# Optimization experiments

Measured on AMD Instinct MI355X. Metric: run time of the kernel, lower is better.

Reference implementation:

```python
import jax, jax.numpy as jnp
import numpy as np

H, D = 16, 1024
HD = D // H  # 64

def setup_inputs() -> dict:
    key = jax.random.key(0)
    ks = jax.random.split(key, 11)
    B, S = 2, 2048
    s_in = 1.0 / np.sqrt(D)
    return {
        "V": jax.random.normal(ks[0], (B, S, D), jnp.float32),
        "K": jax.random.normal(ks[1], (B, S, D), jnp.float32),
        "Q": jax.random.normal(ks[2], (B, S, D), jnp.float32),
        # stacked per-head Linear weights, torch layout [out,in] -> [H, HD, D]
        "Wv": jax.random.normal(ks[3], (H, HD, D), jnp.float32) * s_in,
        "bv": jnp.zeros((H, HD), jnp.float32),
        "Wk": jax.random.normal(ks[4], (H, HD, D), jnp.float32) * s_in,
        "bk": jnp.zeros((H, HD), jnp.float32),
        "Wq": jax.random.normal(ks[5], (H, HD, D), jnp.float32) * s_in,
        "bq": jnp.zeros((H, HD), jnp.float32),
        "Wo": jax.random.normal(ks[6], (D, D), jnp.float32) * s_in,
        "bo": jnp.zeros((D,), jnp.float32),
    }

def reference(V, K, Q, Wv, bv, Wk, bk, Wq, bq, Wo, bo):
    scale = HD ** (-0.5)
    # per-head projections fused into one batched GEMM: [B,S,D] x [H,HD,D] -> [B,H,S,HD]
    q = jnp.einsum('bsd,hed->bhse', Q, Wq) + bq[None, :, None, :]
    k = jnp.einsum('bsd,hed->bhse', K, Wk) + bk[None, :, None, :]
    v = jnp.einsum('bsd,hed->bhse', V, Wv) + bv[None, :, None, :]
    # scaled dot-product attention
    scores = jnp.einsum('bhqe,bhke->bhqk', q, k) * scale  # [B,H,S,S]
    p = jax.nn.softmax(scores, axis=-1)
    att = jnp.einsum('bhqk,bhke->bhqe', p, v)  # [B,H,S,HD]
    # concat heads (head 0 first, matching the torch cat order) then output proj
    B, _, S, _ = att.shape
    cat = jnp.transpose(att, (0, 2, 1, 3)).reshape(B, S, H * HD)
    return cat @ Wo.T + bo
```

## Files before the change

### kernel.cpp

```cpp
#include <hip/hip_runtime.h>
#include <cstdint>
#include <cstddef>

typedef __bf16 bf16_t;
typedef bf16_t bf16x8 __attribute__((ext_vector_type(8)));
typedef bf16_t bf16x4 __attribute__((ext_vector_type(4)));
typedef float f32x4 __attribute__((ext_vector_type(4)));

__device__ __forceinline__ void gl_lds16(const void* g, void* l) {
  __builtin_amdgcn_global_load_lds(
      (const __attribute__((address_space(1))) void*)g,
      (__attribute__((address_space(3))) void*)l, 16, 0, 0);
}

__device__ __forceinline__ f32x4 mfma16(bf16x8 a, bf16x8 b, f32x4 c) {
  return __builtin_amdgcn_mfma_f32_16x16x32_bf16(a, b, c, 0, 0, 0);
}

struct CvtWArgs { const float* src[4]; };

__global__ __launch_bounds__(256) void convert_w(CvtWArgs a, bf16_t* __restrict__ dst) {
  unsigned g = blockIdx.x * 256u + threadIdx.x;
  unsigned seg = g >> 17, off = g & 0x1FFFFu;
  const float4* s = (const float4*)a.src[seg] + (size_t)off * 2;
  float4 x0 = s[0], x1 = s[1];
  bf16x8 o;
  o[0] = (bf16_t)x0.x; o[1] = (bf16_t)x0.y; o[2] = (bf16_t)x0.z; o[3] = (bf16_t)x0.w;
  o[4] = (bf16_t)x1.x; o[5] = (bf16_t)x1.y; o[6] = (bf16_t)x1.z; o[7] = (bf16_t)x1.w;
  *(bf16x8*)(dst + (size_t)g * 8) = o;
}

struct ProjArgs {
  const float* A[3]; const bf16_t* W[3]; const float* bias[3];
  bf16_t* out[3]; float scale[3];
};

__global__ __launch_bounds__(256, 3) void gemm_proj(ProjArgs p) {
  __shared__ __attribute__((aligned(16))) unsigned char smem[36864];
  bf16_t* a_s = (bf16_t*)smem;
  bf16_t* b_s = (bf16_t*)(smem + 16384);
  const int K = 1024;
  const int z = blockIdx.z;
  const float*  A = p.A[z] + (size_t)blockIdx.x * 128 * K;
  const bf16_t* W = p.W[z] + (size_t)blockIdx.y * 128 * K;

  const int t = threadIdx.x;
  const int w = t >> 6, l = t & 63;
  const int lq = l >> 4, lr = l & 15;
  const int mq = w & 1, nq = w >> 1;

  f32x4 acc[4][4];
  f32x4 zero = {0.f, 0.f, 0.f, 0.f};
  #pragma unroll
  for (int i = 0; i < 4; i++)
    #pragma unroll
    for (int j = 0; j < 4; j++) acc[i][j] = zero;

  for (int k0 = 0; k0 < K; k0 += 64) {
    __syncthreads();
    float4 av[8];
    #pragma unroll
    for (int f = 0; f < 8; f++) {
      int g = t + f * 256;
      int r = g >> 4, c16 = g & 15;
      av[f] = *(const float4*)(A + (size_t)r * K + k0 + c16 * 4);
    }
    #pragma unroll
    for (int i = 0; i < 4; i++) {
      int g = t + i * 256;
      int r = g >> 3, pc = g & 7;
      int lc = pc ^ (r & 7);
      gl_lds16(W + (size_t)r * K + k0 + lc * 8, b_s + i * 2048 + w * 512);
    }
    #pragma unroll
    for (int f = 0; f < 8; f++) {
      int g = t + f * 256;
      int r = g >> 4, c16 = g & 15;
      int phys = (c16 >> 1) ^ (r & 7);
      bf16x4 bv;
      bv[0] = (bf16_t)av[f].x; bv[1] = (bf16_t)av[f].y;
      bv[2] = (bf16_t)av[f].z; bv[3] = (bf16_t)av[f].w;
      *(bf16x4*)(a_s + r * 64 + phys * 8 + (c16 & 1) * 4) = bv;
    }
    __syncthreads();
    #pragma unroll
    for (int kk = 0; kk < 2; kk++) {
      bf16x8 af[4], bfr[4];
      #pragma unroll
      for (int i = 0; i < 4; i++) {
        int R = mq * 64 + i * 16 + lr;
        int ch = (kk * 4 + lq) ^ (R & 7);
        af[i] = *(const bf16x8*)(a_s + R * 64 + ch * 8);
      }
      #pragma unroll
      for (int j = 0; j < 4; j++) {
        int R = nq * 64 + j * 16 + lr;
        int ch = (kk * 4 + lq) ^ (R & 7);
        bfr[j] = *(const bf16x8*)(b_s + R * 64 + ch * 8);
      }
      #pragma unroll
      for (int i = 0; i < 4; i++)
        #pragma unroll
        for (int j = 0; j < 4; j++)
          acc[i][j] = mfma16(af[i], bfr[j], acc[i][j]);
    }
  }

  const float* bias = p.bias[z];
  const float scale = p.scale[z];
  __syncthreads();
  bf16_t* ts = (bf16_t*)smem;
  #pragma unroll
  for (int i = 0; i < 4; i++) {
    #pragma unroll
    for (int j = 0; j < 4; j++) {
      int nl = nq * 64 + j * 16 + lr;
      float bz = bias[blockIdx.y * 128 + nl];
      #pragma unroll
      for (int r = 0; r < 4; r++) {
        int ml = mq * 64 + i * 16 + lq * 4 + r;
        bf16_t val = (bf16_t)((acc[i][j][r] + bz) * scale);
        if (z == 0) {
          int mlp = (ml & 96) | (((ml >> 2) & 3) << 3) | (((ml >> 4) & 1) << 2) | (ml & 3);
          ts[nl * 136 + mlp] = val;
        } else {
          ts[ml * 136 + nl] = val;
        }
      }
    }
  }
  __syncthreads();
  bf16_t* out = p.out[z];
  const int b = blockIdx.x >> 4, sbase = (blockIdx.x & 15) * 128;
  if (z == 0) {
    #pragma unroll
    for (int ii = 0; ii < 8; ii++) {
      int idx = t * 8 + ii * 2048;
      int rr = idx >> 7, cc = idx & 127;
      int n = blockIdx.y * 128 + rr;
      int h = n >> 6, e = n & 63;
      bf16x8 vq = *(const bf16x8*)(ts + rr * 136 + cc);
      *(bf16x8*)(out + ((size_t)(b * 16 + h) * 64 + e) * 2048 + sbase + cc) = vq;
    }
  } else {
    #pragma unroll
    for (int ii = 0; ii < 8; ii++) {
      int idx = t * 8 + ii * 2048;
      int rr = idx >> 7, cc = idx & 127;
      int n = blockIdx.y * 128 + cc;
      int h = n >> 6, e = n & 63;
      bf16x8 vq = *(const bf16x8*)(ts + rr * 136 + cc);
      *(bf16x8*)(out + ((size_t)(b * 16 + h) * 2048 + sbase + rr) * 64 + e) = vq;
    }
  }
}

__global__ __launch_bounds__(256, 4) void attn(
    const bf16_t* __restrict__ qw, const bf16_t* __restrict__ kw,
    const bf16_t* __restrict__ vtw, bf16_t* __restrict__ att)
{
  __shared__ bf16_t k_s[64 * 64];
  __shared__ bf16_t v_s[64 * 64];
  __shared__ bf16_t qe_s[64 * 72];
  const int bh = blockIdx.x, qt = blockIdx.y;
  const int t = threadIdx.x, w = t >> 6, l = t & 63, lq = l >> 4, lr = l & 15;

  const bf16_t* qbase = qw + ((size_t)bh * 2048 + qt * 64) * 64;
  #pragma unroll
  for (int i = 0; i < 2; i++) {
    int g = t + i * 256;
    int r = g >> 3, pc = g & 7;
    int lc = pc ^ (r & 7);
    gl_lds16(qbase + (size_t)r * 64 + lc * 8, qe_s + i * 2048 + w * 512);
  }
  __syncthreads();
  bf16x8 qf[2];
  #pragma unroll
  for (int kk = 0; kk < 2; kk++) {
    int R = w * 16 + lr;
    int ch = (kk * 4 + lq) ^ (R & 7);
    qf[kk] = *(const bf16x8*)(qe_s + R * 64 + ch * 8);
  }

  f32x4 O[4];
  f32x4 zero = {0.f, 0.f, 0.f, 0.f};
  #pragma unroll
  for (int et = 0; et < 4; et++) O[et] = zero;
  float lsum = 0.f;

  for (int kt = 0; kt < 32; ++kt) {
    __syncthreads();
    const bf16_t* kbase = kw + ((size_t)bh * 2048 + kt * 64) * 64;
    const bf16_t* vbase = vtw + (size_t)bh * 131072 + (size_t)kt * 64;
    #pragma unroll
    for (int i = 0; i < 2; i++) {
      int g = t + i * 256;
      int r = g >> 3, pc = g & 7;
      int lc = pc ^ (r & 7);
      gl_lds16(kbase + (size_t)r * 64 + lc * 8, k_s + i * 2048 + w * 512);
      gl_lds16(vbase + (size_t)r * 2048 + lc * 8, v_s + i * 2048 + w * 512);
    }
    __syncthreads();

    f32x4 sc[4];
    #pragma unroll
    for (int j = 0; j < 4; j++) sc[j] = zero;
    #pragma unroll
    for (int kk = 0; kk < 2; kk++) {
      #pragma unroll
      for (int j = 0; j < 4; j++) {
        int R = j * 16 + lr;
        int ch = (kk * 4 + lq) ^ (R & 7);
        bf16x8 kf = *(const bf16x8*)(k_s + R * 64 + ch * 8);
        sc[j] = mfma16(kf, qf[kk], sc[j]);
      }
    }

    bf16x8 pb[2];
    #pragma unroll
    for (int ks2 = 0; ks2 < 2; ks2++) {
      #pragma unroll
      for (int r = 0; r < 4; r++) {
        float e0 = __expf(sc[2 * ks2][r]);
        float e1 = __expf(sc[2 * ks2 + 1][r]);
        lsum += e0 + e1;
        pb[ks2][r] = (bf16_t)e0;
        pb[ks2][4 + r] = (bf16_t)e1;
      }
    }

    #pragma unroll
    for (int ks2 = 0; ks2 < 2; ks2++) {
      #pragma unroll
      for (int et = 0; et < 4; et++) {
        int R = et * 16 + lr;
        int ch = (ks2 * 4 + lq) ^ (R & 7);
        bf16x8 vf = *(const bf16x8*)(v_s + R * 64 + ch * 8);
        O[et] = mfma16(vf, pb[ks2], O[et]);
      }
    }
  }

  float s = lsum;
  s += __shfl_xor(s, 16);
  s += __shfl_xor(s, 32);
  float rinv = 1.0f / s;

  #pragma unroll
  for (int et = 0; et < 4; et++) {
    bf16x4 pv;
    #pragma unroll
    for (int r = 0; r < 4; r++) pv[r] = (bf16_t)(O[et][r] * rinv);
    *(bf16x4*)(qe_s + (w * 16 + lr) * 72 + et * 16 + lq * 4) = pv;
  }
  __syncthreads();
  const int b = bh >> 4, h = bh & 15;
  #pragma unroll
  for (int i = 0; i < 2; i++) {
    int c = t + i * 256;
    int row = c >> 3, c8 = c & 7;
    bf16x8 vv = *(const bf16x8*)(qe_s + row * 72 + c8 * 8);
    *(bf16x8*)(att + ((size_t)b * 2048 + qt * 64 + row) * 1024 + h * 64 + c8 * 8) = vv;
  }
}

__global__ __launch_bounds__(256, 2) void gemm_out(
    const bf16_t* __restrict__ A, const bf16_t* __restrict__ W,
    const float* __restrict__ bias, float* __restrict__ out)
{
  __shared__ bf16_t a_s[64 * 64];
  __shared__ bf16_t b_s[128 * 64];
  const int K = 1024;
  const bf16_t* Ab = A + (size_t)blockIdx.x * 64 * K;
  const bf16_t* Wb = W + (size_t)blockIdx.y * 128 * K;
  const int t = threadIdx.x, w = t >> 6, l = t & 63, lq = l >> 4, lr = l & 15;
  const int mh = w & 1, nh = w >> 1;

  f32x4 acc[2][4];
  f32x4 zero = {0.f, 0.f, 0.f, 0.f};
  #pragma unroll
  for (int i = 0; i < 2; i++)
    #pragma unroll
    for (int j = 0; j < 4; j++) acc[i][j] = zero;

  for (int k0 = 0; k0 < K; k0 += 64) {
    __syncthreads();
    #pragma unroll
    for (int i = 0; i < 2; i++) {
      int g = t + i * 256;
      int r = g >> 3, pc = g & 7;
      int lc = pc ^ (r & 7);
      gl_lds16(Ab + (size_t)r * K + k0 + lc * 8, a_s + i * 2048 + w * 512);
    }
    #pragma unroll
    for (int i = 0; i < 4; i++) {
      int g = t + i * 256;
      int r = g >> 3, pc = g & 7;
      int lc = pc ^ (r & 7);
      gl_lds16(Wb + (size_t)r * K + k0 + lc * 8, b_s + i * 2048 + w * 512);
    }
    __syncthreads();
    #pragma unroll
    for (int kk = 0; kk < 2; kk++) {
      bf16x8 af[2], bfr[4];
      #pragma unroll
      for (int i = 0; i < 2; i++) {
        int R = mh * 32 + i * 16 + lr;
        int ch = (kk * 4 + lq) ^ (R & 7);
        af[i] = *(const bf16x8*)(a_s + R * 64 + ch * 8);
      }
      #pragma unroll
      for (int j = 0; j < 4; j++) {
        int R = nh * 64 + j * 16 + lr;
        int ch = (kk * 4 + lq) ^ (R & 7);
        bfr[j] = *(const bf16x8*)(b_s + R * 64 + ch * 8);
      }
      #pragma unroll
      for (int i = 0; i < 2; i++)
        #pragma unroll
        for (int j = 0; j < 4; j++)
          acc[i][j] = mfma16(af[i], bfr[j], acc[i][j]);
    }
  }

  #pragma unroll
  for (int i = 0; i < 2; i++) {
    #pragma unroll
    for (int j = 0; j < 4; j++) {
      int col = blockIdx.y * 128 + nh * 64 + j * 16 + lr;
      float bz = bias[col];
      #pragma unroll
      for (int r = 0; r < 4; r++) {
        int row = blockIdx.x * 64 + mh * 32 + i * 16 + lq * 4 + r;
        out[(size_t)row * 1024 + col] = acc[i][j][r] + bz;
      }
    }
  }
}

extern "C" void kernel_launch(void* const* d_in, const int* in_sizes, int n_in,
                              void* d_out, int out_size, void* d_ws, size_t ws_size,
                              hipStream_t stream) {
  (void)in_sizes; (void)n_in; (void)out_size;
  const float* V  = (const float*)d_in[0];
  const float* Kx = (const float*)d_in[1];
  const float* Q  = (const float*)d_in[2];
  const float* Wv = (const float*)d_in[3];
  const float* bv = (const float*)d_in[4];
  const float* Wk = (const float*)d_in[5];
  const float* bk = (const float*)d_in[6];
  const float* Wq = (const float*)d_in[7];
  const float* bq = (const float*)d_in[8];
  const float* Wo = (const float*)d_in[9];
  const float* bo = (const float*)d_in[10];

  const size_t E = 1048576;
  if (ws_size < 20 * E * sizeof(bf16_t)) return;

  bf16_t* ws = (bf16_t*)d_ws;
  bf16_t* cWo   = ws;
  bf16_t* cWv   = ws + E;
  bf16_t* cWk   = ws + 2 * E;
  bf16_t* cWq   = ws + 3 * E;
  bf16_t* q_ws  = ws + 4 * E;
  bf16_t* k_ws  = ws + 8 * E;
  bf16_t* vt_ws = ws + 12 * E;
  bf16_t* att_ws= ws + 16 * E;

  CvtWArgs cw;
  cw.src[0] = Wo; cw.src[1] = Wv; cw.src[2] = Wk; cw.src[3] = Wq;
  convert_w<<<2048, 256, 0, stream>>>(cw, ws);

  ProjArgs pa;
  pa.A[0] = V;   pa.A[1] = Kx;  pa.A[2] = Q;
  pa.W[0] = cWv; pa.W[1] = cWk; pa.W[2] = cWq;
  pa.bias[0] = bv; pa.bias[1] = bk; pa.bias[2] = bq;
  pa.out[0] = vt_ws; pa.out[1] = k_ws; pa.out[2] = q_ws;
  pa.scale[0] = 1.f; pa.scale[1] = 1.f; pa.scale[2] = 0.125f;
  gemm_proj<<<dim3(32, 8, 3), 256, 0, stream>>>(pa);

  attn<<<dim3(32, 32), 256, 0, stream>>>(q_ws, k_ws, vt_ws, att_ws);

  gemm_out<<<dim3(64, 8), 256, 0, stream>>>(att_ws, cWo, bo, (float*)d_out);
}
```

Before: 216.0 us.

## Double-buffer LDS staging in all GEMM/attention kernels and pre-convert activations to bf16

Pre-converts V, K, Q activations to bf16 in one combined conversion kernel, storing them in the att workspace and the output buffer as scratch. This lets the projection GEMM stage A via direct global-to-LDS loads. The projection, attention and output GEMM loops now double-buffer LDS, prefetching the next tile while computing the current one, with raw barriers, explicit waitcnt and s_setprio around MFMA. The extra conversion pass adds memory traffic, and the larger LDS footprint changes occupancy (proj drops to 2 blocks, out rises to 3).

```diff
diff --git a/kernel.cpp b/kernel.cpp
--- a/kernel.cpp
+++ b/kernel.cpp
@@ -17,32 +17,59 @@
   return __builtin_amdgcn_mfma_f32_16x16x32_bf16(a, b, c, 0, 0, 0);
 }
 
-struct CvtWArgs { const float* src[4]; };
-
-__global__ __launch_bounds__(256) void convert_w(CvtWArgs a, bf16_t* __restrict__ dst) {
+#define SCHED_FENCE() __builtin_amdgcn_sched_barrier(0)
+#define WAIT_VM0()   do { asm volatile("s_waitcnt vmcnt(0)");   SCHED_FENCE(); } while (0)
+#define WAIT_LGKM0() do { asm volatile("s_waitcnt lgkmcnt(0)"); SCHED_FENCE(); } while (0)
+#define RAW_BAR()    do { __builtin_amdgcn_s_barrier();         SCHED_FENCE(); } while (0)
+
+struct CvtArgs { const float* src[7]; bf16_t* dst[7]; };
+
+__global__ __launch_bounds__(256) void convert_all(CvtArgs a) {
   unsigned g = blockIdx.x * 256u + threadIdx.x;
-  unsigned seg = g >> 17, off = g & 0x1FFFFu;
+  unsigned seg, off;
+  if (g < 524288u) {
+    seg = g >> 17; off = g & 131071u;
+  } else {
+    unsigned h = g - 524288u;
+    seg = 4u + (h >> 19); off = h & 524287u;
+  }
   const float4* s = (const float4*)a.src[seg] + (size_t)off * 2;
   float4 x0 = s[0], x1 = s[1];
   bf16x8 o;
   o[0] = (bf16_t)x0.x; o[1] = (bf16_t)x0.y; o[2] = (bf16_t)x0.z; o[3] = (bf16_t)x0.w;
   o[4] = (bf16_t)x1.x; o[5] = (bf16_t)x1.y; o[6] = (bf16_t)x1.z; o[7] = (bf16_t)x1.w;
-  *(bf16x8*)(dst + (size_t)g * 8) = o;
+  *(bf16x8*)(a.dst[seg] + (size_t)off * 8) = o;
+}
+
+__device__ __forceinline__ void stage128(const bf16_t* src, bf16_t* dst, int t, int w) {
+  #pragma unroll
+  for (int i = 0; i < 4; i++) {
+    int g = t + i * 256;
+    int r = g >> 3, pc = g & 7;
+    int lc = pc ^ (r & 7);
+    gl_lds16(src + (size_t)r * 1024 + lc * 8, dst + i * 2048 + w * 512);
+  }
+}
+__device__ __forceinline__ void stage64(const bf16_t* src, bf16_t* dst, int t, int w) {
+  #pragma unroll
+  for (int i = 0; i < 2; i++) {
+    int g = t + i * 256;
+    int r = g >> 3, pc = g & 7;
+    int lc = pc ^ (r & 7);
+    gl_lds16(src + (size_t)r * 1024 + lc * 8, dst + i * 2048 + w * 512);
+  }
 }
 
 struct ProjArgs {
-  const float* A[3]; const bf16_t* W[3]; const float* bias[3];
+  const bf16_t* A[3]; const bf16_t* W[3]; const float* bias[3];
   bf16_t* out[3]; float scale[3];
 };
 
-__global__ __launch_bounds__(256, 3) void gemm_proj(ProjArgs p) {
-  __shared__ __attribute__((aligned(16))) unsigned char smem[36864];
-  bf16_t* a_s = (bf16_t*)smem;
-  bf16_t* b_s = (bf16_t*)(smem + 16384);
-  const int K = 1024;
+__global__ __launch_bounds__(256, 2) void gemm_proj(ProjArgs p) {
+  __shared__ __attribute__((aligned(16))) unsigned char smem[65536];
   const int z = blockIdx.z;
-  const float*  A = p.A[z] + (size_t)blockIdx.x * 128 * K;
-  const bf16_t* W = p.W[z] + (size_t)blockIdx.y * 128 * K;
+  const bf16_t* A = p.A[z] + (size_t)blockIdx.x * 128 * 1024;
+  const bf16_t* W = p.W[z] + (size_t)blockIdx.y * 128 * 1024;
 
   const int t = threadIdx.x;
   const int w = t >> 6, l = t & 63;
@@ -56,33 +83,21 @@
     #pragma unroll
     for (int j = 0; j < 4; j++) acc[i][j] = zero;
 
-  for (int k0 = 0; k0 < K; k0 += 64) {
-    __syncthreads();
-    float4 av[8];
-    #pragma unroll
-    for (int f = 0; f < 8; f++) {
-      int g = t + f * 256;
-      int r = g >> 4, c16 = g & 15;
-      av[f] = *(const float4*)(A + (size_t)r * K + k0 + c16 * 4);
-    }
-    #pragma unroll
-    for (int i = 0; i < 4; i++) {
-      int g = t + i * 256;
-      int r = g >> 3, pc = g & 7;
-      int lc = pc ^ (r & 7);
-      gl_lds16(W + (size_t)r * K + k0 + lc * 8, b_s + i * 2048 + w * 512);
-    }
-    #pragma unroll
-    for (int f = 0; f < 8; f++) {
-      int g = t + f * 256;
-      int r = g >> 4, c16 = g & 15;
-      int phys = (c16 >> 1) ^ (r & 7);
-      bf16x4 bv;
-      bv[0] = (bf16_t)av[f].x; bv[1] = (bf16_t)av[f].y;
-      bv[2] = (bf16_t)av[f].z; bv[3] = (bf16_t)av[f].w;
-      *(bf16x4*)(a_s + r * 64 + phys * 8 + (c16 & 1) * 4) = bv;
-    }
-    __syncthreads();
+  stage128(A, (bf16_t*)smem, t, w);
+  stage128(W, (bf16_t*)(smem + 16384), t, w);
+  WAIT_VM0();
+  RAW_BAR();
+
+  for (int step = 0; step < 16; ++step) {
+    const int cur = step & 1;
+    bf16_t* as = (bf16_t*)(smem + cur * 32768);
+    bf16_t* bs = (bf16_t*)(smem + cur * 32768 + 16384);
+    if (step < 15) {
+      bf16_t* an = (bf16_t*)(smem + (cur ^ 1) * 32768);
+      stage128(A + (step + 1) * 64, an, t, w);
+      stage128(W + (step + 1) * 64, an + 8192, t, w);
+    }
+    SCHED_FENCE();
     #pragma unroll
     for (int kk = 0; kk < 2; kk++) {
       bf16x8 af[4], bfr[4];
@@ -90,20 +105,24 @@
       for (int i = 0; i < 4; i++) {
         int R = mq * 64 + i * 16 + lr;
         int ch = (kk * 4 + lq) ^ (R & 7);
-        af[i] = *(const bf16x8*)(a_s + R * 64 + ch * 8);
+        af[i] = *(const bf16x8*)(as + R * 64 + ch * 8);
       }
       #pragma unroll
       for (int j = 0; j < 4; j++) {
         int R = nq * 64 + j * 16 + lr;
         int ch = (kk * 4 + lq) ^ (R & 7);
-        bfr[j] = *(const bf16x8*)(b_s + R * 64 + ch * 8);
-      }
+        bfr[j] = *(const bf16x8*)(bs + R * 64 + ch * 8);
+      }
+      __builtin_amdgcn_s_setprio(1);
       #pragma unroll
       for (int i = 0; i < 4; i++)
         #pragma unroll
         for (int j = 0; j < 4; j++)
           acc[i][j] = mfma16(af[i], bfr[j], acc[i][j]);
-    }
+      __builtin_amdgcn_s_setprio(0);
+    }
+    WAIT_VM0();
+    RAW_BAR();
   }
 
   const float* bias = p.bias[z];
@@ -159,11 +178,13 @@
     const bf16_t* __restrict__ qw, const bf16_t* __restrict__ kw,
     const bf16_t* __restrict__ vtw, bf16_t* __restrict__ att)
 {
-  __shared__ bf16_t k_s[64 * 64];
-  __shared__ bf16_t v_s[64 * 64];
-  __shared__ bf16_t qe_s[64 * 72];
+  __shared__ __attribute__((aligned(16))) unsigned char smem[32768];
+  bf16_t* qe_s = (bf16_t*)(smem + 16384);
   const int bh = blockIdx.x, qt = blockIdx.y;
   const int t = threadIdx.x, w = t >> 6, l = t & 63, lq = l >> 4, lr = l & 15;
+
+  const bf16_t* kb0 = kw + (size_t)bh * 131072;
+  const bf16_t* vb0 = vtw + (size_t)bh * 131072;
 
   const bf16_t* qbase = qw + ((size_t)bh * 2048 + qt * 64) * 64;
   #pragma unroll
@@ -172,8 +193,11 @@
     int r = g >> 3, pc = g & 7;
     int lc = pc ^ (r & 7);
     gl_lds16(qbase + (size_t)r * 64 + lc * 8, qe_s + i * 2048 + w * 512);
-  }
-  __syncthreads();
+    gl_lds16(kb0 + (size_t)r * 64 + lc * 8, (bf16_t*)smem + i * 2048 + w * 512);
+    gl_lds16(vb0 + (size_t)r * 2048 + lc * 8, (bf16_t*)(smem + 8192) + i * 2048 + w * 512);
+  }
+  WAIT_VM0();
+  RAW_BAR();
   bf16x8 qf[2];
   #pragma unroll
   for (int kk = 0; kk < 2; kk++) {
@@ -181,6 +205,8 @@
     int ch = (kk * 4 + lq) ^ (R & 7);
     qf[kk] = *(const bf16x8*)(qe_s + R * 64 + ch * 8);
   }
+  WAIT_LGKM0();
+  RAW_BAR();
 
   f32x4 O[4];
   f32x4 zero = {0.f, 0.f, 0.f, 0.f};
@@ -189,18 +215,23 @@
   float lsum = 0.f;
 
   for (int kt = 0; kt < 32; ++kt) {
-    __syncthreads();
-    const bf16_t* kbase = kw + ((size_t)bh * 2048 + kt * 64) * 64;
-    const bf16_t* vbase = vtw + (size_t)bh * 131072 + (size_t)kt * 64;
-    #pragma unroll
-    for (int i = 0; i < 2; i++) {
-      int g = t + i * 256;
-      int r = g >> 3, pc = g & 7;
-      int lc = pc ^ (r & 7);
-      gl_lds16(kbase + (size_t)r * 64 + lc * 8, k_s + i * 2048 + w * 512);
-      gl_lds16(vbase + (size_t)r * 2048 + lc * 8, v_s + i * 2048 + w * 512);
-    }
-    __syncthreads();
+    const int cur = kt & 1;
+    bf16_t* ks = (bf16_t*)(smem + cur * 16384);
+    bf16_t* vs = (bf16_t*)(smem + cur * 16384 + 8192);
+    if (kt < 31) {
+      bf16_t* kn = (bf16_t*)(smem + (cur ^ 1) * 16384);
+      const bf16_t* kbase = kb0 + (size_t)(kt + 1) * 64 * 64;
+      const bf16_t* vbase = vb0 + (size_t)(kt + 1) * 64;
+      #pragma unroll
+      for (int i = 0; i < 2; i++) {
+        int g = t + i * 256;
+        int r = g >> 3, pc = g & 7;
+        int lc = pc ^ (r & 7);
+        gl_lds16(kbase + (size_t)r * 64 + lc * 8, kn + i * 2048 + w * 512);
+        gl_lds16(vbase + (size_t)r * 2048 + lc * 8, kn + 4096 + i * 2048 + w * 512);
+      }
+    }
+    SCHED_FENCE();
 
     f32x4 sc[4];
     #pragma unroll
@@ -211,8 +242,10 @@
       for (int j = 0; j < 4; j++) {
         int R = j * 16 + lr;
         int ch = (kk * 4 + lq) ^ (R & 7);
-        bf16x8 kf = *(const bf16x8*)(k_s + R * 64 + ch * 8);
+        bf16x8 kf = *(const bf16x8*)(ks + R * 64 + ch * 8);
+        __builtin_amdgcn_s_setprio(1);
         sc[j] = mfma16(kf, qf[kk], sc[j]);
+        __builtin_amdgcn_s_setprio(0);
       }
     }
 
@@ -235,10 +268,14 @@
       for (int et = 0; et < 4; et++) {
         int R = et * 16 + lr;
         int ch = (ks2 * 4 + lq) ^ (R & 7);
-        bf16x8 vf = *(const bf16x8*)(v_s + R * 64 + ch * 8);
+        bf16x8 vf = *(const bf16x8*)(vs + R * 64 + ch * 8);
+        __builtin_amdgcn_s_setprio(1);
         O[et] = mfma16(vf, pb[ks2], O[et]);
-      }
-    }
+        __builtin_amdgcn_s_setprio(0);
+      }
+    }
+    WAIT_VM0();
+    RAW_BAR();
   }
 
   float s = lsum;
@@ -264,15 +301,13 @@
   }
 }
 
-__global__ __launch_bounds__(256, 2) void gemm_out(
+__global__ __launch_bounds__(256, 3) void gemm_out(
     const bf16_t* __restrict__ A, const bf16_t* __restrict__ W,
     const float* __restrict__ bias, float* __restrict__ out)
 {
-  __shared__ bf16_t a_s[64 * 64];
-  __shared__ bf16_t b_s[128 * 64];
-  const int K = 1024;
-  const bf16_t* Ab = A + (size_t)blockIdx.x * 64 * K;
-  const bf16_t* Wb = W + (size_t)blockIdx.y * 128 * K;
+  __shared__ __attribute__((aligned(16))) unsigned char smem[49152];
+  const bf16_t* Ab = A + (size_t)blockIdx.x * 64 * 1024;
+  const bf16_t* Wb = W + (size_t)blockIdx.y * 128 * 1024;
   const int t = threadIdx.x, w = t >> 6, l = t & 63, lq = l >> 4, lr = l & 15;
   const int mh = w & 1, nh = w >> 1;
 
@@ -283,23 +318,21 @@
     #pragma unroll
     for (int j = 0; j < 4; j++) acc[i][j] = zero;
 
-  for (int k0 = 0; k0 < K; k0 += 64) {
-    __syncthreads();
-    #pragma unroll
-    for (int i = 0; i < 2; i++) {
-      int g = t + i * 256;
-      int r = g >> 3, pc = g & 7;
-      int lc = pc ^ (r & 7);
-      gl_lds16(Ab + (size_t)r * K + k0 + lc * 8, a_s + i * 2048 + w * 512);
-    }
-    #pragma unroll
-    for (int i = 0; i < 4; i++) {
-      int g = t + i * 256;
-      int r = g >> 3, pc = g & 7;
-      int lc = pc ^ (r & 7);
-      gl_lds16(Wb + (size_t)r * K + k0 + lc * 8, b_s + i * 2048 + w * 512);
-    }
-    __syncthreads();
+  stage64(Ab, (bf16_t*)smem, t, w);
+  stage128(Wb, (bf16_t*)(smem + 8192), t, w);
+  WAIT_VM0();
+  RAW_BAR();
+
+  for (int step = 0; step < 16; ++step) {
+    const int cur = step & 1;
+    bf16_t* as = (bf16_t*)(smem + cur * 24576);
+    bf16_t* bs = (bf16_t*)(smem + cur * 24576 + 8192);
+    if (step < 15) {
+      bf16_t* an = (bf16_t*)(smem + (cur ^ 1) * 24576);
+      stage64(Ab + (step + 1) * 64, an, t, w);
+      stage128(Wb + (step + 1) * 64, an + 4096, t, w);
+    }
+    SCHED_FENCE();
     #pragma unroll
     for (int kk = 0; kk < 2; kk++) {
       bf16x8 af[2], bfr[4];
@@ -307,20 +340,24 @@
       for (int i = 0; i < 2; i++) {
         int R = mh * 32 + i * 16 + lr;
         int ch = (kk * 4 + lq) ^ (R & 7);
-        af[i] = *(const bf16x8*)(a_s + R * 64 + ch * 8);
+        af[i] = *(const bf16x8*)(as + R * 64 + ch * 8);
       }
       #pragma unroll
       for (int j = 0; j < 4; j++) {
         int R = nh * 64 + j * 16 + lr;
         int ch = (kk * 4 + lq) ^ (R & 7);
-        bfr[j] = *(const bf16x8*)(b_s + R * 64 + ch * 8);
-      }
+        bfr[j] = *(const bf16x8*)(bs + R * 64 + ch * 8);
+      }
+      __builtin_amdgcn_s_setprio(1);
       #pragma unroll
       for (int i = 0; i < 2; i++)
         #pragma unroll
         for (int j = 0; j < 4; j++)
           acc[i][j] = mfma16(af[i], bfr[j], acc[i][j]);
-    }
+      __builtin_amdgcn_s_setprio(0);
+    }
+    WAIT_VM0();
+    RAW_BAR();
   }
 
   #pragma unroll
@@ -367,12 +404,19 @@
   bf16_t* vt_ws = ws + 12 * E;
   bf16_t* att_ws= ws + 16 * E;
 
-  CvtWArgs cw;
-  cw.src[0] = Wo; cw.src[1] = Wv; cw.src[2] = Wk; cw.src[3] = Wq;
-  convert_w<<<2048, 256, 0, stream>>>(cw, ws);
+  bf16_t* cV = att_ws;
+  bf16_t* cK = (bf16_t*)d_out;
+  bf16_t* cQ = (bf16_t*)d_out + 4 * E;
+
+  CvtArgs ca;
+  ca.src[0] = Wo; ca.src[1] = Wv; ca.src[2] = Wk; ca.src[3] = Wq;
+  ca.src[4] = V;  ca.src[5] = Kx; ca.src[6] = Q;
+  ca.dst[0] = cWo; ca.dst[1] = cWv; ca.dst[2] = cWk; ca.dst[3] = cWq;
+  ca.dst[4] = cV;  ca.dst[5] = cK;  ca.dst[6] = cQ;
+  convert_all<<<8192, 256, 0, stream>>>(ca);
 
   ProjArgs pa;
-  pa.A[0] = V;   pa.A[1] = Kx;  pa.A[2] = Q;
+  pa.A[0] = cV;  pa.A[1] = cK;  pa.A[2] = cQ;
   pa.W[0] = cWv; pa.W[1] = cWk; pa.W[2] = cWq;
   pa.bias[0] = bv; pa.bias[1] = bk; pa.bias[2] = bq;
   pa.out[0] = vt_ws; pa.out[1] = k_ws; pa.out[2] = q_ws;
```

Measured after the change: 207.4 us. 1.04x faster.
